# Optimization experiments

Hardware: AMD Instinct MI355X
Metric: run time of the kernel (lower is better)

Reference implementation:

```python
import jax, jax.numpy as jnp
import numpy as np

B, N, OBS_DIM = 64, 512, 128
HIDDEN_DIM, MESSAGE_DIM, ACTION_DIM = 256, 128, 16


def _dense_params(key, din, dout):
    kw, kb = jax.random.split(key)
    W = jax.random.normal(kw, (din, dout), jnp.float32) * 0.02
    b = jnp.zeros((dout,), jnp.float32)
    return W, b


def setup_inputs() -> dict:
    key = jax.random.key(0)
    ks = jax.random.split(key, 12)
    obs_batch = jax.random.normal(ks[0], (B, N, OBS_DIM), jnp.float32)
    dones_batch = jnp.zeros((B, N), jnp.bool_)
    We, be = _dense_params(ks[1], OBS_DIM, HIDDEN_DIM)
    Wc, bc = _dense_params(ks[2], HIDDEN_DIM, MESSAGE_DIM // 4)
    Wn, bn = _dense_params(ks[3], HIDDEN_DIM, MESSAGE_DIM // 2)
    Wb, bb = _dense_params(ks[4], HIDDEN_DIM, MESSAGE_DIM // 4)
    Wi, bi = _dense_params(ks[5], HIDDEN_DIM, 1)
    Wq, bq = _dense_params(ks[6], HIDDEN_DIM, MESSAGE_DIM)
    Wk, bk = _dense_params(ks[7], MESSAGE_DIM, MESSAGE_DIM)
    Wv, bv = _dense_params(ks[8], MESSAGE_DIM, MESSAGE_DIM)
    Wp, bp = _dense_params(ks[9], HIDDEN_DIM + MESSAGE_DIM, HIDDEN_DIM)
    Wa, ba = _dense_params(ks[10], HIDDEN_DIM, ACTION_DIM)
    Wcr, bcr = _dense_params(ks[11], HIDDEN_DIM, 1)
    return {"obs_batch": obs_batch, "dones_batch": dones_batch,
            "We": We, "be": be, "Wc": Wc, "bc": bc, "Wn": Wn, "bn": bn,
            "Wb": Wb, "bb": bb, "Wi": Wi, "bi": bi, "Wq": Wq, "bq": bq,
            "Wk": Wk, "bk": bk, "Wv": Wv, "bv": bv, "Wp": Wp, "bp": bp,
            "Wa": Wa, "ba": ba, "Wcr": Wcr, "bcr": bcr}


def reference(obs_batch, dones_batch, We, be, Wc, bc, Wn, bn, Wb, bb, Wi, bi,
              Wq, bq, Wk, bk, Wv, bv, Wp, bp, Wa, ba, Wcr, bcr):
    dense = lambda x, W, b: x @ W + b
    encoded = jax.nn.relu(dense(obs_batch, We, be))                 # [B,N,H]
    messages = jnp.concatenate([dense(encoded, Wc, bc),
                                dense(encoded, Wn, bn),
                                dense(encoded, Wb, bb)], axis=-1)   # [B,N,M]
    importance = jax.nn.sigmoid(dense(encoded, Wi, bi))             # [B,N,1]
    Q = dense(encoded, Wq, bq)
    K = dense(messages, Wk, bk)
    V = dense(messages, Wv, bv)
    scores = jnp.einsum('bqd,bkd->bqk', Q, K) / jnp.sqrt(jnp.float32(MESSAGE_DIM))
    importance_weights = importance * jnp.transpose(importance, (0, 2, 1))  # [B,N,N]
    scores = scores * importance_weights
    norms = jnp.linalg.norm(obs_batch, axis=-1, keepdims=True)      # [B,N,1]
    obs_sim = jnp.einsum('bid,bjd->bij', obs_batch, obs_batch)
    obs_sim = obs_sim / (norms + 1e-08)
    obs_sim = obs_sim / (jnp.transpose(norms, (0, 2, 1)) + 1e-08)
    scores = scores + obs_sim * 0.5
    attn = jax.nn.softmax(scores, axis=-1)
    aggregated = jnp.einsum('bqk,bkd->bqd', attn, V)                # [B,N,M]
    combined = jnp.concatenate([encoded, aggregated], axis=-1)
    x = jax.nn.relu(dense(combined, Wp, bp))
    logits = dense(x, Wa, ba)
    value = dense(x, Wcr, bcr).squeeze(-1)
    return (logits, value)
```

## Files before the change

kernel.cpp:

```cpp
#include <hip/hip_runtime.h>
#include <math.h>


typedef __attribute__((ext_vector_type(8))) short short8;
typedef __attribute__((ext_vector_type(4))) float f32x4;

#define RSQRT_D 0.08838834764831843f
#define MFMA __builtin_amdgcn_mfma_f32_16x16x32_bf16

__device__ __forceinline__ unsigned short f2bf(float f) {
  union { float f; unsigned u; } v; v.f = f;
  return (unsigned short)((v.u + 0x7FFFu + ((v.u >> 16) & 1u)) >> 16);
}
__device__ __forceinline__ float bf2f(unsigned short h) {
  union { unsigned u; float f; } v; v.u = ((unsigned)h) << 16;
  return v.f;
}
__device__ __forceinline__ unsigned pack2(float a, float b) {
  return (unsigned)f2bf(a) | ((unsigned)f2bf(b) << 16);
}
__device__ __forceinline__ short8 ld8(const unsigned short* p) {
  return *(const short8*)p;
}
__device__ __forceinline__ void gl16(const unsigned short* g,
                                     unsigned short* l) {
  __builtin_amdgcn_global_load_lds(
      (const __attribute__((address_space(1))) unsigned int*)(const void*)g,
      (__attribute__((address_space(3))) unsigned int*)(void*)l, 16, 0, 0);
}

__global__ __launch_bounds__(256) void prep_all(
    const float* __restrict__ obs, const float* __restrict__ We,
    const float* __restrict__ Wq, const float* __restrict__ Wk,
    const float* __restrict__ Wv, const float* __restrict__ Wp,
    const float* __restrict__ Wc, const float* __restrict__ Wn,
    const float* __restrict__ Wb, const float* __restrict__ bc,
    const float* __restrict__ bn, const float* __restrict__ bb,
    const float* __restrict__ Wa, const float* __restrict__ Wcr,
    const float* __restrict__ ba, const float* __restrict__ bcr,
    const float* __restrict__ bq, unsigned short* __restrict__ WeT,
    unsigned short* __restrict__ Wqkv, unsigned short* __restrict__ Wkv,
    unsigned short* __restrict__ Wm_nt, unsigned short* __restrict__ WpT,
    unsigned short* __restrict__ WaCrT, float* __restrict__ bm,
    float* __restrict__ bqkv, unsigned short* __restrict__ obs_bf,
    unsigned short* __restrict__ As, unsigned short* __restrict__ Bs,
    float* __restrict__ logits, float* __restrict__ value,
    float* __restrict__ imp_raw) {
  const int bid = blockIdx.x, tid = threadIdx.x;
  if (bid < 929) {
    int idx = bid * 256 + tid;
    if (idx < 32768) {
      int n = idx >> 7, k = idx & 127;
      WeT[idx] = f2bf(We[k * 256 + n]);
    } else if (idx < 65536) {
      int i = idx - 32768;
      int n = i >> 8, k = i & 255;
      Wqkv[i] = f2bf(Wq[k * 128 + n]);
    } else if (idx < 98304) {
      int i = idx - 65536;
      int n = i >> 7, k = i & 127;
      Wkv[i] = f2bf(n < 128 ? Wk[k * 128 + n] : Wv[k * 128 + (n - 128)]);
    } else if (idx < 131072) {
      int i = idx - 98304;
      int h = i >> 7, m = i & 127;
      float v = (m < 32)   ? Wc[h * 32 + m]
              : (m < 96)   ? Wn[h * 64 + (m - 32)]
                           : Wb[h * 32 + (m - 96)];
      Wm_nt[i] = f2bf(v);
    } else if (idx < 229376) {
      int i = idx - 131072;
      int n = i / 384, k = i - n * 384;
      WpT[i] = f2bf(Wp[k * 256 + n]);
    } else if (idx < 237568) {
      int i = idx - 229376;
      int n = i >> 8, k = i & 255;
      float v = (n < 16) ? Wa[k * 16 + n] : (n == 16) ? Wcr[k] : 0.f;
      WaCrT[i] = f2bf(v);
    } else if (idx < 237696) {
      int i = idx - 237568;
      bm[i] = (i < 32) ? bc[i] : (i < 96) ? bn[i - 32] : bb[i - 96];
    } else if (idx < 237824) {
      int i = idx - 237696;
      bqkv[i] = bq[i];
    }
  } else if (bid < 2977) {
    const int wave = tid >> 6, lane = tid & 63;
    const int t0 = (bid - 929) * 16 + wave * 4;
#pragma unroll
    for (int it = 0; it < 4; ++it) {
      int t = t0 + it;
      const float* row = obs + (size_t)t * 128;
      float2 o = *(const float2*)(row + lane * 2);
      float s2 = o.x * o.x + o.y * o.y;
#pragma unroll
      for (int off = 1; off < 64; off <<= 1) s2 += __shfl_xor(s2, off);
      float inv = 1.f / (sqrtf(s2) + 1e-8f);
      ((unsigned*)obs_bf)[(size_t)t * 64 + lane] = pack2(o.x, o.y);
      ((unsigned*)As)[(size_t)t * 128 + 64 + lane] =
          pack2(o.x * 0.5f * inv, o.y * 0.5f * inv);
      ((unsigned*)Bs)[(size_t)t * 128 + 64 + lane] =
          pack2(o.x * inv, o.y * inv);
    }
  } else if (bid < 5153) {
    int i = (bid - 2977) * 256 + tid;
    if (i < 524288) logits[i] = ba[i & 15];
    else value[i - 524288] = bcr[0];
  } else {
    imp_raw[(bid - 5153) * 256 + tid] = 0.f;
  }
}

__global__ __launch_bounds__(256) void prep_wprod(
    const unsigned short* __restrict__ Wkv,
    const unsigned short* __restrict__ Wm_nt, const float* __restrict__ bm,
    const float* __restrict__ bk, const float* __restrict__ bv,
    unsigned short* __restrict__ Wqkv, float* __restrict__ bqkv) {
  const int bid = blockIdx.x, tid = threadIdx.x;
  if (bid < 8) {
    const int lane = tid & 63, wave = tid >> 6;
    const int quad = lane >> 4, l16 = lane & 15;
    const int r0 = bid * 32;
    f32x4 acc[2][4];
#pragma unroll
    for (int i = 0; i < 2; ++i)
#pragma unroll
      for (int j = 0; j < 4; ++j) acc[i][j] = (f32x4){0.f, 0.f, 0.f, 0.f};
#pragma unroll
    for (int kc = 0; kc < 4; ++kc) {
      short8 af[2], bf[4];
#pragma unroll
      for (int i = 0; i < 2; ++i)
        af[i] = ld8(Wkv + (size_t)(r0 + i * 16 + l16) * 128 + kc * 32 + quad * 8);
#pragma unroll
      for (int j = 0; j < 4; ++j)
        bf[j] = ld8(Wm_nt + (size_t)(wave * 64 + j * 16 + l16) * 128 + kc * 32 +
                    quad * 8);
#pragma unroll
      for (int i = 0; i < 2; ++i)
#pragma unroll
        for (int j = 0; j < 4; ++j)
          acc[i][j] = MFMA(af[i], bf[j], acc[i][j], 0, 0, 0);
    }
#pragma unroll
    for (int i = 0; i < 2; ++i) {
      const int row = r0 + i * 16 + quad * 4;
#pragma unroll
      for (int j = 0; j < 4; ++j) {
        const int col = wave * 64 + j * 16 + l16;
#pragma unroll
        for (int r = 0; r < 4; ++r)
          Wqkv[(size_t)(128 + row + r) * 256 + col] = f2bf(acc[i][j][r]);
      }
    }
  } else {
    int i = tid;
    float acc = (i < 128) ? bk[i] : bv[i - 128];
    for (int m = 0; m < 128; ++m)
      acc += bm[m] * bf2f(Wkv[(size_t)i * 128 + m]);
    bqkv[128 + i] = acc;
  }
}

__global__ __launch_bounds__(256, 2) void enc_gemm(
    const unsigned short* __restrict__ obs_bf,
    const unsigned short* __restrict__ WeT, const float* __restrict__ be,
    const float* __restrict__ Wi, unsigned short* __restrict__ enc,
    float* __restrict__ imp_raw) {
  __shared__ unsigned short Asr[16384];
  __shared__ unsigned short Bsr[16384];
  const int tid = threadIdx.x, lane = tid & 63, wave = tid >> 6;
  const int quad = lane >> 4, l16 = lane & 15;
  const int wm = wave & 1, wn = wave >> 1;
  const int bm0 = blockIdx.y * 128, bn0 = blockIdx.x * 128;

#pragma unroll
  for (int it = 0; it < 8; ++it) {
    int c = it * 256 + tid;
    int row = c >> 4, ch = c & 15;
    gl16(obs_bf + (size_t)(bm0 + row) * 128 + ((ch ^ (row & 15)) << 3),
         Asr + it * 2048 + wave * 512);
    gl16(WeT + (size_t)(bn0 + row) * 128 + ((ch ^ (row & 15)) << 3),
         Bsr + it * 2048 + wave * 512);
  }
  __syncthreads();

  f32x4 acc[4][4];
#pragma unroll
  for (int i = 0; i < 4; ++i)
#pragma unroll
    for (int j = 0; j < 4; ++j) acc[i][j] = (f32x4){0.f, 0.f, 0.f, 0.f};
#pragma unroll
  for (int ks = 0; ks < 4; ++ks) {
    short8 af[4], bf[4];
#pragma unroll
    for (int mi = 0; mi < 4; ++mi) {
      int row = wm * 64 + mi * 16 + l16;
      af[mi] = *(const short8*)&Asr[row * 128 + (((ks * 4 + quad) ^ (row & 15)) << 3)];
    }
#pragma unroll
    for (int ni = 0; ni < 4; ++ni) {
      int row = wn * 64 + ni * 16 + l16;
      bf[ni] = *(const short8*)&Bsr[row * 128 + (((ks * 4 + quad) ^ (row & 15)) << 3)];
    }
#pragma unroll
    for (int mi = 0; mi < 4; ++mi)
#pragma unroll
      for (int ni = 0; ni < 4; ++ni)
        acc[mi][ni] = MFMA(af[mi], bf[ni], acc[mi][ni], 0, 0, 0);
  }

#pragma unroll
  for (int mi = 0; mi < 4; ++mi) {
    const int rowb = bm0 + wm * 64 + mi * 16 + quad * 4;
    float ip[4] = {0.f, 0.f, 0.f, 0.f};
#pragma unroll
    for (int ni = 0; ni < 4; ++ni) {
      const int col = bn0 + wn * 64 + ni * 16 + l16;
      const float bvv = be[col], wv = Wi[col];
#pragma unroll
      for (int r = 0; r < 4; ++r) {
        float v = fmaxf(acc[mi][ni][r] + bvv, 0.f);
        enc[(size_t)(rowb + r) * 256 + col] = f2bf(v);
        ip[r] += v * wv;
      }
    }
#pragma unroll
    for (int r = 0; r < 4; ++r) {
#pragma unroll
      for (int off = 1; off < 16; off <<= 1) ip[r] += __shfl_xor(ip[r], off);
    }
    if (l16 == 0) {
#pragma unroll
      for (int r = 0; r < 4; ++r) atomicAdd(&imp_raw[rowb + r], ip[r]);
    }
  }
}

__global__ __launch_bounds__(256, 2) void qkv_gemm(
    const unsigned short* __restrict__ enc, const unsigned short* __restrict__ Wqkv,
    const float* __restrict__ bqkv, const float* __restrict__ imp_raw,
    const float* __restrict__ bi, unsigned short* __restrict__ As,
    unsigned short* __restrict__ Bs, unsigned short* __restrict__ vT) {
  __shared__ unsigned short Asr[8192];
  __shared__ unsigned short Bsr[8192];
  const int tid = threadIdx.x, lane = tid & 63, wave = tid >> 6;
  const int quad = lane >> 4, l16 = lane & 15;
  const int wm = wave & 1, wn = wave >> 1;
  const int bx = blockIdx.x;
  const int bm0 = blockIdx.y * 128, bn0 = bx * 128;
  const int srow = tid >> 3, slc = tid & 7;

  f32x4 acc[4][4];
#pragma unroll
  for (int i = 0; i < 4; ++i)
#pragma unroll
    for (int j = 0; j < 4; ++j) acc[i][j] = (f32x4){0.f, 0.f, 0.f, 0.f};

  for (int kt = 0; kt < 256; kt += 64) {
#pragma unroll
    for (int i = 0; i < 4; ++i) {
      int row = i * 32 + srow;
      gl16(enc + (size_t)(bm0 + row) * 256 + kt + ((slc ^ (row & 7)) << 3),
           Asr + i * 2048 + wave * 512);
      gl16(Wqkv + (size_t)(bn0 + row) * 256 + kt + ((slc ^ (row & 7)) << 3),
           Bsr + i * 2048 + wave * 512);
    }
    __syncthreads();
#pragma unroll
    for (int ks = 0; ks < 2; ++ks) {
      short8 af[4], bf[4];
#pragma unroll
      for (int mi = 0; mi < 4; ++mi) {
        int row = wm * 64 + mi * 16 + l16;
        af[mi] = *(const short8*)&Asr[row * 64 + (((ks * 4 + quad) ^ (row & 7)) << 3)];
      }
#pragma unroll
      for (int ni = 0; ni < 4; ++ni) {
        int row = wn * 64 + ni * 16 + l16;
        bf[ni] = *(const short8*)&Bsr[row * 64 + (((ks * 4 + quad) ^ (row & 7)) << 3)];
      }
#pragma unroll
      for (int mi = 0; mi < 4; ++mi)
#pragma unroll
        for (int ni = 0; ni < 4; ++ni)
          acc[mi][ni] = MFMA(af[mi], bf[ni], acc[mi][ni], 0, 0, 0);
    }
    __syncthreads();
  }

  const float bi0 = bi[0];
#pragma unroll
  for (int mi = 0; mi < 4; ++mi) {
    const int rowb = bm0 + wm * 64 + mi * 16 + quad * 4;
    float sg[4];
    if (bx < 2) {
      const float mult = (bx == 0) ? RSQRT_D : 1.0f;
#pragma unroll
      for (int r = 0; r < 4; ++r)
        sg[r] = mult / (1.f + __expf(-(imp_raw[rowb + r] + bi0)));
    }
#pragma unroll
    for (int ni = 0; ni < 4; ++ni) {
      const int col = wn * 64 + ni * 16 + l16;
      const float bvv = bqkv[bx * 128 + col];
      if (bx == 0) {
#pragma unroll
        for (int r = 0; r < 4; ++r)
          As[(size_t)(rowb + r) * 256 + col] = f2bf((acc[mi][ni][r] + bvv) * sg[r]);
      } else if (bx == 1) {
#pragma unroll
        for (int r = 0; r < 4; ++r)
          Bs[(size_t)(rowb + r) * 256 + col] = f2bf((acc[mi][ni][r] + bvv) * sg[r]);
      } else {
        uint2 o;
        o.x = pack2(acc[mi][ni][0] + bvv, acc[mi][ni][1] + bvv);
        o.y = pack2(acc[mi][ni][2] + bvv, acc[mi][ni][3] + bvv);
        *(uint2*)(vT + ((size_t)(rowb >> 9) * 128 + col) * 512 + (rowb & 511)) = o;
      }
    }
  }
}

__global__ __launch_bounds__(512, 4) void flash4b(
    const unsigned short* __restrict__ As, const unsigned short* __restrict__ Bs,
    const unsigned short* __restrict__ vT, unsigned short* __restrict__ agg) {
  __shared__ unsigned short Ub[16384];
  __shared__ unsigned short Pp[8192];
  __shared__ float redm[2][64];
  __shared__ float reds[2][64];
  const int tid = threadIdx.x, lane = tid & 63, wave = tid >> 6;
  const int quad = lane >> 4, l16 = lane & 15;
  const int wm = wave & 3, wn = wave >> 2;
  const int b = blockIdx.x & 63;
  const int qt = blockIdx.x >> 6;
  const size_t tok0 = (size_t)b * 512 + qt * 64;
  const int srow = tid >> 4, slc = tid & 15;

  short8 af[8];
#pragma unroll
  for (int kc = 0; kc < 8; ++kc)
    af[kc] = ld8(As + (tok0 + wm * 16 + l16) * 256 + kc * 32 + quad * 8);

  f32x4 s[4][4];
#pragma unroll
  for (int kt = 0; kt < 4; ++kt)
#pragma unroll
    for (int nt = 0; nt < 4; ++nt) s[kt][nt] = (f32x4){0.f, 0.f, 0.f, 0.f};

#pragma unroll
  for (int kt = 0; kt < 4; ++kt) {
#pragma unroll
    for (int kh = 0; kh < 2; ++kh) {
      __syncthreads();
#pragma unroll
      for (int i = 0; i < 4; ++i) {
        int row = i * 32 + srow;
        gl16(Bs + ((size_t)b * 512 + kt * 128 + row) * 256 + kh * 128 +
                 ((slc ^ (row & 15)) << 3),
             Ub + i * 4096 + wave * 512);
      }
      __syncthreads();
#pragma unroll
      for (int kk = 0; kk < 4; ++kk) {
        short8 bfr[4];
#pragma unroll
        for (int nt = 0; nt < 4; ++nt) {
          int rr = wn * 64 + nt * 16 + l16;
          bfr[nt] = *(const short8*)&Ub[rr * 128 + (((kk * 4 + quad) ^ (rr & 15)) << 3)];
        }
#pragma unroll
        for (int nt = 0; nt < 4; ++nt)
          s[kt][nt] = MFMA(af[kh * 4 + kk], bfr[nt], s[kt][nt], 0, 0, 0);
      }
    }
  }

  const int rbase = wm * 16 + quad * 4;
  float mt[4];
#pragma unroll
  for (int r = 0; r < 4; ++r) {
    float mv = -1e30f;
#pragma unroll
    for (int kt = 0; kt < 4; ++kt)
#pragma unroll
      for (int nt = 0; nt < 4; ++nt) mv = fmaxf(mv, s[kt][nt][r]);
#pragma unroll
    for (int off = 1; off < 16; off <<= 1) mv = fmaxf(mv, __shfl_xor(mv, off));
    mt[r] = mv;
  }
  if (l16 == 0) {
#pragma unroll
    for (int r = 0; r < 4; ++r) redm[wn][rbase + r] = mt[r];
  }
  __syncthreads();
  float lsum[4];
#pragma unroll
  for (int r = 0; r < 4; ++r) {
    float mfull = fmaxf(mt[r], redm[1 ^ wn][rbase + r]);
    float sum = 0.f;
#pragma unroll
    for (int kt = 0; kt < 4; ++kt)
#pragma unroll
      for (int nt = 0; nt < 4; ++nt) {
        float p = __expf(s[kt][nt][r] - mfull);
        s[kt][nt][r] = p;
        sum += p;
      }
#pragma unroll
    for (int off = 1; off < 16; off <<= 1) sum += __shfl_xor(sum, off);
    lsum[r] = sum;
  }
  if (l16 == 0) {
#pragma unroll
    for (int r = 0; r < 4; ++r) reds[wn][rbase + r] = lsum[r];
  }
  __syncthreads();
  float linv[4];
#pragma unroll
  for (int r = 0; r < 4; ++r)
    linv[r] = 1.0f / (lsum[r] + reds[1 ^ wn][rbase + r]);

  f32x4 oacc[4];
#pragma unroll
  for (int nt = 0; nt < 4; ++nt) oacc[nt] = (f32x4){0.f, 0.f, 0.f, 0.f};
#pragma unroll
  for (int vt = 0; vt < 4; ++vt) {
    __syncthreads();
#pragma unroll
    for (int nt = 0; nt < 4; ++nt) {
      const int col = wn * 64 + nt * 16 + l16;
#pragma unroll
      for (int r = 0; r < 4; ++r) {
        const int row = rbase + r;
        Pp[row * 128 + (((col >> 3) ^ (row & 15)) << 3) + (col & 7)] =
            f2bf(s[vt][nt][r]);
      }
    }
#pragma unroll
    for (int i = 0; i < 4; ++i) {
      int row = i * 32 + srow;
      gl16(vT + ((size_t)b * 128 + row) * 512 + vt * 128 +
               ((slc ^ (row & 15)) << 3),
           Ub + i * 4096 + wave * 512);
    }
    __syncthreads();
#pragma unroll
    for (int kk = 0; kk < 4; ++kk) {
      const int prow = wm * 16 + l16;
      short8 pa = *(const short8*)&Pp[prow * 128 + (((kk * 4 + quad) ^ (prow & 15)) << 3)];
#pragma unroll
      for (int nt = 0; nt < 4; ++nt) {
        int rr = wn * 64 + nt * 16 + l16;
        short8 vb = *(const short8*)&Ub[rr * 128 + (((kk * 4 + quad) ^ (rr & 15)) << 3)];
        oacc[nt] = MFMA(pa, vb, oacc[nt], 0, 0, 0);
      }
    }
  }
#pragma unroll
  for (int nt = 0; nt < 4; ++nt) {
    const int col = wn * 64 + nt * 16 + l16;
#pragma unroll
    for (int r = 0; r < 4; ++r)
      agg[(tok0 + rbase + r) * 128 + col] = f2bf(oacc[nt][r] * linv[r]);
  }
}

__global__ __launch_bounds__(256, 2) void xh_gemm(
    const unsigned short* __restrict__ enc, const unsigned short* __restrict__ agg,
    const unsigned short* __restrict__ WpT, const float* __restrict__ bp,
    const unsigned short* __restrict__ WaCrT, float* __restrict__ logits,
    float* __restrict__ value) {
  __shared__ unsigned short sm[16384];
  unsigned short* Asr = sm;
  unsigned short* Bsr = sm + 8192;
  const int tid = threadIdx.x, lane = tid & 63, wave = tid >> 6;
  const int quad = lane >> 4, l16 = lane & 15;
  const int wm = wave & 1, wn = wave >> 1;
  const int bm = blockIdx.y * 128, bn = blockIdx.x * 128;
  const int srow = tid >> 3, slc = tid & 7;

  f32x4 acc[4][4];
#pragma unroll
  for (int i = 0; i < 4; ++i)
#pragma unroll
    for (int j = 0; j < 4; ++j) acc[i][j] = (f32x4){0.f, 0.f, 0.f, 0.f};

  for (int kt = 0; kt < 384; kt += 64) {
    const unsigned short* Ap;
    int lda, kloc;
    if (kt < 256) { Ap = enc; lda = 256; kloc = kt; }
    else          { Ap = agg; lda = 128; kloc = kt - 256; }
#pragma unroll
    for (int i = 0; i < 4; ++i) {
      int row = i * 32 + srow;
      gl16(Ap + (size_t)(bm + row) * lda + kloc + ((slc ^ (row & 7)) << 3),
           Asr + i * 2048 + wave * 512);
      gl16(WpT + (size_t)(bn + row) * 384 + kt + ((slc ^ (row & 7)) << 3),
           Bsr + i * 2048 + wave * 512);
    }
    __syncthreads();
#pragma unroll
    for (int ks = 0; ks < 2; ++ks) {
      short8 af[4], bf[4];
#pragma unroll
      for (int mi = 0; mi < 4; ++mi) {
        int row = wm * 64 + mi * 16 + l16;
        af[mi] = *(const short8*)&Asr[row * 64 + (((ks * 4 + quad) ^ (row & 7)) << 3)];
      }
#pragma unroll
      for (int ni = 0; ni < 4; ++ni) {
        int row = wn * 64 + ni * 16 + l16;
        bf[ni] = *(const short8*)&Bsr[row * 64 + (((ks * 4 + quad) ^ (row & 7)) << 3)];
      }
#pragma unroll
      for (int mi = 0; mi < 4; ++mi)
#pragma unroll
        for (int ni = 0; ni < 4; ++ni)
          acc[mi][ni] = MFMA(af[mi], bf[ni], acc[mi][ni], 0, 0, 0);
    }
    __syncthreads();
  }

#pragma unroll
  for (int mi = 0; mi < 4; ++mi) {
    const int row = wm * 64 + mi * 16 + quad * 4;
#pragma unroll
    for (int ni = 0; ni < 4; ++ni) {
      const int colc = wn * 64 + ni * 16 + l16;
      const float bv = bp[bn + colc];
#pragma unroll
      for (int r = 0; r < 4; ++r) {
        float v = fmaxf(acc[mi][ni][r] + bv, 0.f);
        sm[(row + r) * 128 + (((colc >> 3) ^ ((row + r) & 15)) << 3) + (colc & 7)] =
            f2bf(v);
      }
    }
  }
  __syncthreads();

  f32x4 h[2][2];
#pragma unroll
  for (int i = 0; i < 2; ++i)
#pragma unroll
    for (int j = 0; j < 2; ++j) h[i][j] = (f32x4){0.f, 0.f, 0.f, 0.f};
#pragma unroll
  for (int kc = 0; kc < 4; ++kc) {
    short8 xa[2], wb[2];
#pragma unroll
    for (int hm = 0; hm < 2; ++hm) {
      int row = wave * 32 + hm * 16 + l16;
      xa[hm] = *(const short8*)&sm[row * 128 + (((kc * 4 + quad) ^ (row & 15)) << 3)];
    }
#pragma unroll
    for (int hn = 0; hn < 2; ++hn)
      wb[hn] = ld8(WaCrT + (size_t)(hn * 16 + l16) * 256 + bn + kc * 32 + quad * 8);
#pragma unroll
    for (int hm = 0; hm < 2; ++hm)
#pragma unroll
      for (int hn = 0; hn < 2; ++hn)
        h[hm][hn] = MFMA(xa[hm], wb[hn], h[hm][hn], 0, 0, 0);
  }
#pragma unroll
  for (int hm = 0; hm < 2; ++hm) {
#pragma unroll
    for (int hn = 0; hn < 2; ++hn) {
      const int n = hn * 16 + l16;
#pragma unroll
      for (int r = 0; r < 4; ++r) {
        const int grow = bm + wave * 32 + hm * 16 + quad * 4 + r;
        if (n < 16)
          atomicAdd(&logits[(size_t)grow * 16 + n], h[hm][hn][r]);
        else if (n == 16)
          atomicAdd(&value[grow], h[hm][hn][r]);
      }
    }
  }
}

extern "C" void kernel_launch(void* const* d_in, const int* in_sizes, int n_in,
                              void* d_out, int out_size, void* d_ws,
                              size_t ws_size, hipStream_t stream) {
  const float* obs = (const float*)d_in[0];
  const float* We = (const float*)d_in[2];
  const float* be = (const float*)d_in[3];
  const float* Wc = (const float*)d_in[4];
  const float* bc = (const float*)d_in[5];
  const float* Wn = (const float*)d_in[6];
  const float* bn = (const float*)d_in[7];
  const float* Wb = (const float*)d_in[8];
  const float* bb = (const float*)d_in[9];
  const float* Wi = (const float*)d_in[10];
  const float* bi = (const float*)d_in[11];
  const float* Wq = (const float*)d_in[12];
  const float* bq = (const float*)d_in[13];
  const float* Wk = (const float*)d_in[14];
  const float* bk = (const float*)d_in[15];
  const float* Wv = (const float*)d_in[16];
  const float* bv = (const float*)d_in[17];
  const float* Wp = (const float*)d_in[18];
  const float* bp = (const float*)d_in[19];
  const float* Wa = (const float*)d_in[20];
  const float* ba = (const float*)d_in[21];
  const float* Wcr = (const float*)d_in[22];
  const float* bcr = (const float*)d_in[23];

  char* base = (char*)d_ws;
  unsigned short* enc_bf = (unsigned short*)(base);
  unsigned short* As     = (unsigned short*)(base + 16777216);
  unsigned short* Bs     = (unsigned short*)(base + 33554432);
  unsigned short* obsagg = (unsigned short*)(base + 50331648);
  unsigned short* vT     = (unsigned short*)(base + 58720256);
  float* imp_raw         = (float*)(base + 67108864);
  unsigned short* WeT    = (unsigned short*)(base + 67239936);
  unsigned short* Wqkv   = (unsigned short*)(base + 67305472);
  unsigned short* Wkv    = (unsigned short*)(base + 67502080);
  unsigned short* Wm_nt  = (unsigned short*)(base + 67567616);
  unsigned short* WpT    = (unsigned short*)(base + 67633152);
  unsigned short* WaCrT  = (unsigned short*)(base + 67829760);
  float* bmb             = (float*)(base + 67846144);
  float* bqkv            = (float*)(base + 67846656);

  float* logits = (float*)d_out;
  float* value = (float*)d_out + 524288;

  prep_all<<<5281, 256, 0, stream>>>(obs, We, Wq, Wk, Wv, Wp, Wc, Wn, Wb, bc,
                                     bn, bb, Wa, Wcr, ba, bcr, bq, WeT, Wqkv,
                                     Wkv, Wm_nt, WpT, WaCrT, bmb, bqkv, obsagg,
                                     As, Bs, logits, value, imp_raw);
  prep_wprod<<<9, 256, 0, stream>>>(Wkv, Wm_nt, bmb, bk, bv, Wqkv, bqkv);

  enc_gemm<<<dim3(2, 256), 256, 0, stream>>>(obsagg, WeT, be, Wi, enc_bf,
                                             imp_raw);
  qkv_gemm<<<dim3(3, 256), 256, 0, stream>>>(enc_bf, Wqkv, bqkv, imp_raw, bi,
                                             As, Bs, vT);
  flash4b<<<512, 512, 0, stream>>>(As, Bs, vT, obsagg);
  xh_gemm<<<dim3(2, 256), 256, 0, stream>>>(enc_bf, obsagg, WpT, bp, WaCrT,
                                            logits, value);
}
```

Baseline: 183.5 us.

## Merge weight-product prep into encoder kernel and double-buffer GEMM K-loops

```diff
diff --git a/kernel.cpp b/kernel.cpp
--- a/kernel.cpp
+++ b/kernel.cpp
@@ -110,68 +110,71 @@
   }
 }
 
-__global__ __launch_bounds__(256) void prep_wprod(
-    const unsigned short* __restrict__ Wkv,
-    const unsigned short* __restrict__ Wm_nt, const float* __restrict__ bm,
-    const float* __restrict__ bk, const float* __restrict__ bv,
-    unsigned short* __restrict__ Wqkv, float* __restrict__ bqkv) {
-  const int bid = blockIdx.x, tid = threadIdx.x;
-  if (bid < 8) {
-    const int lane = tid & 63, wave = tid >> 6;
-    const int quad = lane >> 4, l16 = lane & 15;
-    const int r0 = bid * 32;
-    f32x4 acc[2][4];
-#pragma unroll
-    for (int i = 0; i < 2; ++i)
-#pragma unroll
-      for (int j = 0; j < 4; ++j) acc[i][j] = (f32x4){0.f, 0.f, 0.f, 0.f};
-#pragma unroll
-    for (int kc = 0; kc < 4; ++kc) {
-      short8 af[2], bf[4];
-#pragma unroll
-      for (int i = 0; i < 2; ++i)
-        af[i] = ld8(Wkv + (size_t)(r0 + i * 16 + l16) * 128 + kc * 32 + quad * 8);
-#pragma unroll
-      for (int j = 0; j < 4; ++j)
-        bf[j] = ld8(Wm_nt + (size_t)(wave * 64 + j * 16 + l16) * 128 + kc * 32 +
-                    quad * 8);
-#pragma unroll
-      for (int i = 0; i < 2; ++i)
-#pragma unroll
-        for (int j = 0; j < 4; ++j)
-          acc[i][j] = MFMA(af[i], bf[j], acc[i][j], 0, 0, 0);
-    }
-#pragma unroll
-    for (int i = 0; i < 2; ++i) {
-      const int row = r0 + i * 16 + quad * 4;
-#pragma unroll
-      for (int j = 0; j < 4; ++j) {
-        const int col = wave * 64 + j * 16 + l16;
-#pragma unroll
-        for (int r = 0; r < 4; ++r)
-          Wqkv[(size_t)(128 + row + r) * 256 + col] = f2bf(acc[i][j][r]);
-      }
-    }
-  } else {
-    int i = tid;
-    float acc = (i < 128) ? bk[i] : bv[i - 128];
-    for (int m = 0; m < 128; ++m)
-      acc += bm[m] * bf2f(Wkv[(size_t)i * 128 + m]);
-    bqkv[128 + i] = acc;
-  }
-}
-
-__global__ __launch_bounds__(256, 2) void enc_gemm(
+__global__ __launch_bounds__(256, 2) void enc_wprod(
     const unsigned short* __restrict__ obs_bf,
     const unsigned short* __restrict__ WeT, const float* __restrict__ be,
     const float* __restrict__ Wi, unsigned short* __restrict__ enc,
-    float* __restrict__ imp_raw) {
+    float* __restrict__ imp_raw, const unsigned short* __restrict__ Wkv,
+    const unsigned short* __restrict__ Wm_nt, const float* __restrict__ bmc,
+    const float* __restrict__ bk, const float* __restrict__ bv,
+    unsigned short* __restrict__ Wqkv, float* __restrict__ bqkv) {
   __shared__ unsigned short Asr[16384];
   __shared__ unsigned short Bsr[16384];
-  const int tid = threadIdx.x, lane = tid & 63, wave = tid >> 6;
+  const int bid = blockIdx.x, tid = threadIdx.x;
+
+  if (bid >= 512) {
+    const int wb = bid - 512;
+    if (wb < 8) {
+      const int lane = tid & 63, wave = tid >> 6;
+      const int quad = lane >> 4, l16 = lane & 15;
+      const int r0 = wb * 32;
+      f32x4 acc[2][4];
+#pragma unroll
+      for (int i = 0; i < 2; ++i)
+#pragma unroll
+        for (int j = 0; j < 4; ++j) acc[i][j] = (f32x4){0.f, 0.f, 0.f, 0.f};
+#pragma unroll
+      for (int kc = 0; kc < 4; ++kc) {
+        short8 af[2], bf[4];
+#pragma unroll
+        for (int i = 0; i < 2; ++i)
+          af[i] =
+              ld8(Wkv + (size_t)(r0 + i * 16 + l16) * 128 + kc * 32 + quad * 8);
+#pragma unroll
+        for (int j = 0; j < 4; ++j)
+          bf[j] = ld8(Wm_nt + (size_t)(wave * 64 + j * 16 + l16) * 128 +
+                      kc * 32 + quad * 8);
+#pragma unroll
+        for (int i = 0; i < 2; ++i)
+#pragma unroll
+          for (int j = 0; j < 4; ++j)
+            acc[i][j] = MFMA(af[i], bf[j], acc[i][j], 0, 0, 0);
+      }
+#pragma unroll
+      for (int i = 0; i < 2; ++i) {
+        const int row = r0 + i * 16 + quad * 4;
+#pragma unroll
+        for (int j = 0; j < 4; ++j) {
+          const int col = wave * 64 + j * 16 + l16;
+#pragma unroll
+          for (int r = 0; r < 4; ++r)
+            Wqkv[(size_t)(128 + row + r) * 256 + col] = f2bf(acc[i][j][r]);
+        }
+      }
+    } else {
+      int i = tid;
+      float acc = (i < 128) ? bk[i] : bv[i - 128];
+      for (int m = 0; m < 128; ++m)
+        acc += bmc[m] * bf2f(Wkv[(size_t)i * 128 + m]);
+      bqkv[128 + i] = acc;
+    }
+    return;
+  }
+
+  const int lane = tid & 63, wave = tid >> 6;
   const int quad = lane >> 4, l16 = lane & 15;
   const int wm = wave & 1, wn = wave >> 1;
-  const int bm0 = blockIdx.y * 128, bn0 = blockIdx.x * 128;
+  const int bm0 = (bid >> 1) * 128, bn0 = (bid & 1) * 128;
 
 #pragma unroll
   for (int it = 0; it < 8; ++it) {
@@ -248,7 +251,7 @@
   const int wm = wave & 1, wn = wave >> 1;
   const int bx = blockIdx.x;
   const int bm0 = blockIdx.y * 128, bn0 = bx * 128;
-  const int srow = tid >> 3, slc = tid & 7;
+  const int sr4 = tid >> 2, sl4 = tid & 3;
 
   f32x4 acc[4][4];
 #pragma unroll
@@ -256,35 +259,40 @@
 #pragma unroll
     for (int j = 0; j < 4; ++j) acc[i][j] = (f32x4){0.f, 0.f, 0.f, 0.f};
 
-  for (int kt = 0; kt < 256; kt += 64) {
-#pragma unroll
-    for (int i = 0; i < 4; ++i) {
-      int row = i * 32 + srow;
-      gl16(enc + (size_t)(bm0 + row) * 256 + kt + ((slc ^ (row & 7)) << 3),
-           Asr + i * 2048 + wave * 512);
-      gl16(Wqkv + (size_t)(bn0 + row) * 256 + kt + ((slc ^ (row & 7)) << 3),
-           Bsr + i * 2048 + wave * 512);
-    }
-    __syncthreads();
-#pragma unroll
-    for (int ks = 0; ks < 2; ++ks) {
-      short8 af[4], bf[4];
-#pragma unroll
-      for (int mi = 0; mi < 4; ++mi) {
-        int row = wm * 64 + mi * 16 + l16;
-        af[mi] = *(const short8*)&Asr[row * 64 + (((ks * 4 + quad) ^ (row & 7)) << 3)];
-      }
-#pragma unroll
-      for (int ni = 0; ni < 4; ++ni) {
-        int row = wn * 64 + ni * 16 + l16;
-        bf[ni] = *(const short8*)&Bsr[row * 64 + (((ks * 4 + quad) ^ (row & 7)) << 3)];
-      }
-#pragma unroll
-      for (int mi = 0; mi < 4; ++mi)
-#pragma unroll
-        for (int ni = 0; ni < 4; ++ni)
-          acc[mi][ni] = MFMA(af[mi], bf[ni], acc[mi][ni], 0, 0, 0);
-    }
+  auto stage = [&](int t, int bo) {
+#pragma unroll
+    for (int i = 0; i < 2; ++i) {
+      int row = i * 64 + sr4;
+      int col = t * 32 + ((sl4 ^ (row & 3)) << 3);
+      gl16(enc + (size_t)(bm0 + row) * 256 + col,
+           Asr + bo + i * 2048 + wave * 512);
+      gl16(Wqkv + (size_t)(bn0 + row) * 256 + col,
+           Bsr + bo + i * 2048 + wave * 512);
+    }
+  };
+
+  stage(0, 0);
+  __syncthreads();
+#pragma unroll 8
+  for (int t = 0; t < 8; ++t) {
+    if (t < 7) stage(t + 1, ((t + 1) & 1) * 4096);
+    const int bo = (t & 1) * 4096;
+    short8 af[4], bf[4];
+#pragma unroll
+    for (int mi = 0; mi < 4; ++mi) {
+      int row = wm * 64 + mi * 16 + l16;
+      af[mi] = *(const short8*)&Asr[bo + row * 32 + ((quad ^ (row & 3)) << 3)];
+    }
+#pragma unroll
+    for (int ni = 0; ni < 4; ++ni) {
+      int row = wn * 64 + ni * 16 + l16;
+      bf[ni] = *(const short8*)&Bsr[bo + row * 32 + ((quad ^ (row & 3)) << 3)];
+    }
+#pragma unroll
+    for (int mi = 0; mi < 4; ++mi)
+#pragma unroll
+      for (int ni = 0; ni < 4; ++ni)
+        acc[mi][ni] = MFMA(af[mi], bf[ni], acc[mi][ni], 0, 0, 0);
     __syncthreads();
   }
 
@@ -335,6 +343,7 @@
   const int qt = blockIdx.x >> 6;
   const size_t tok0 = (size_t)b * 512 + qt * 64;
   const int srow = tid >> 4, slc = tid & 15;
+  const int qr8 = tid >> 3, ql8 = tid & 7;
 
   short8 af[8];
 #pragma unroll
@@ -347,32 +356,37 @@
 #pragma unroll
     for (int nt = 0; nt < 4; ++nt) s[kt][nt] = (f32x4){0.f, 0.f, 0.f, 0.f};
 
-#pragma unroll
-  for (int kt = 0; kt < 4; ++kt) {
-#pragma unroll
-    for (int kh = 0; kh < 2; ++kh) {
-      __syncthreads();
-#pragma unroll
-      for (int i = 0; i < 4; ++i) {
-        int row = i * 32 + srow;
-        gl16(Bs + ((size_t)b * 512 + kt * 128 + row) * 256 + kh * 128 +
-                 ((slc ^ (row & 15)) << 3),
-             Ub + i * 4096 + wave * 512);
-      }
-      __syncthreads();
-#pragma unroll
-      for (int kk = 0; kk < 4; ++kk) {
-        short8 bfr[4];
-#pragma unroll
-        for (int nt = 0; nt < 4; ++nt) {
-          int rr = wn * 64 + nt * 16 + l16;
-          bfr[nt] = *(const short8*)&Ub[rr * 128 + (((kk * 4 + quad) ^ (rr & 15)) << 3)];
-        }
-#pragma unroll
-        for (int nt = 0; nt < 4; ++nt)
-          s[kt][nt] = MFMA(af[kh * 4 + kk], bfr[nt], s[kt][nt], 0, 0, 0);
-      }
-    }
+  auto qstage = [&](int c) {
+    const int kt_ = c >> 2, dq_ = c & 3;
+#pragma unroll
+    for (int r2 = 0; r2 < 2; ++r2) {
+      int row = r2 * 64 + qr8;
+      gl16(Bs + ((size_t)b * 512 + kt_ * 128 + row) * 256 + dq_ * 64 +
+               ((ql8 ^ (row & 7)) << 3),
+           Ub + (c & 1) * 8192 + r2 * 4096 + wave * 512);
+    }
+  };
+  qstage(0);
+  __syncthreads();
+#pragma unroll 16
+  for (int c = 0; c < 16; ++c) {
+    if (c < 15) qstage(c + 1);
+    const int kt = c >> 2, dq = c & 3;
+    const int ub0 = (c & 1) * 8192;
+#pragma unroll
+    for (int kk2 = 0; kk2 < 2; ++kk2) {
+      short8 bfr[4];
+#pragma unroll
+      for (int nt = 0; nt < 4; ++nt) {
+        int rr = wn * 64 + nt * 16 + l16;
+        bfr[nt] = *(const short8*)&Ub[ub0 + rr * 64 +
+                                      (((kk2 * 2 + quad) ^ (rr & 7)) << 3)];
+      }
+#pragma unroll
+      for (int nt = 0; nt < 4; ++nt)
+        s[kt][nt] = MFMA(af[dq * 2 + kk2], bfr[nt], s[kt][nt], 0, 0, 0);
+    }
+    __syncthreads();
   }
 
   const int rbase = wm * 16 + quad * 4;
@@ -477,7 +491,7 @@
   const int quad = lane >> 4, l16 = lane & 15;
   const int wm = wave & 1, wn = wave >> 1;
   const int bm = blockIdx.y * 128, bn = blockIdx.x * 128;
-  const int srow = tid >> 3, slc = tid & 7;
+  const int sr4 = tid >> 2, sl4 = tid & 3;
 
   f32x4 acc[4][4];
 #pragma unroll
@@ -485,39 +499,44 @@
 #pragma unroll
     for (int j = 0; j < 4; ++j) acc[i][j] = (f32x4){0.f, 0.f, 0.f, 0.f};
 
-  for (int kt = 0; kt < 384; kt += 64) {
+  auto stage = [&](int t, int bo) {
     const unsigned short* Ap;
-    int lda, kloc;
-    if (kt < 256) { Ap = enc; lda = 256; kloc = kt; }
-    else          { Ap = agg; lda = 128; kloc = kt - 256; }
-#pragma unroll
-    for (int i = 0; i < 4; ++i) {
-      int row = i * 32 + srow;
-      gl16(Ap + (size_t)(bm + row) * lda + kloc + ((slc ^ (row & 7)) << 3),
-           Asr + i * 2048 + wave * 512);
-      gl16(WpT + (size_t)(bn + row) * 384 + kt + ((slc ^ (row & 7)) << 3),
-           Bsr + i * 2048 + wave * 512);
-    }
-    __syncthreads();
-#pragma unroll
-    for (int ks = 0; ks < 2; ++ks) {
-      short8 af[4], bf[4];
-#pragma unroll
-      for (int mi = 0; mi < 4; ++mi) {
-        int row = wm * 64 + mi * 16 + l16;
-        af[mi] = *(const short8*)&Asr[row * 64 + (((ks * 4 + quad) ^ (row & 7)) << 3)];
-      }
-#pragma unroll
-      for (int ni = 0; ni < 4; ++ni) {
-        int row = wn * 64 + ni * 16 + l16;
-        bf[ni] = *(const short8*)&Bsr[row * 64 + (((ks * 4 + quad) ^ (row & 7)) << 3)];
-      }
-#pragma unroll
-      for (int mi = 0; mi < 4; ++mi)
-#pragma unroll
-        for (int ni = 0; ni < 4; ++ni)
-          acc[mi][ni] = MFMA(af[mi], bf[ni], acc[mi][ni], 0, 0, 0);
-    }
+    int lda, kc;
+    if (t < 8) { Ap = enc; lda = 256; kc = t * 32; }
+    else       { Ap = agg; lda = 128; kc = t * 32 - 256; }
+#pragma unroll
+    for (int i = 0; i < 2; ++i) {
+      int row = i * 64 + sr4;
+      int sw = (sl4 ^ (row & 3)) << 3;
+      gl16(Ap + (size_t)(bm + row) * lda + kc + sw,
+           Asr + bo + i * 2048 + wave * 512);
+      gl16(WpT + (size_t)(bn + row) * 384 + t * 32 + sw,
+           Bsr + bo + i * 2048 + wave * 512);
+    }
+  };
+
+  stage(0, 0);
+  __syncthreads();
+#pragma unroll 12
+  for (int t = 0; t < 12; ++t) {
+    if (t < 11) stage(t + 1, ((t + 1) & 1) * 4096);
+    const int bo = (t & 1) * 4096;
+    short8 af[4], bf[4];
+#pragma unroll
+    for (int mi = 0; mi < 4; ++mi) {
+      int row = wm * 64 + mi * 16 + l16;
+      af[mi] = *(const short8*)&Asr[bo + row * 32 + ((quad ^ (row & 3)) << 3)];
+    }
+#pragma unroll
+    for (int ni = 0; ni < 4; ++ni) {
+      int row = wn * 64 + ni * 16 + l16;
+      bf[ni] = *(const short8*)&Bsr[bo + row * 32 + ((quad ^ (row & 3)) << 3)];
+    }
+#pragma unroll
+    for (int mi = 0; mi < 4; ++mi)
+#pragma unroll
+      for (int ni = 0; ni < 4; ++ni)
+        acc[mi][ni] = MFMA(af[mi], bf[ni], acc[mi][ni], 0, 0, 0);
     __syncthreads();
   }
 
@@ -627,10 +646,8 @@
                                      bn, bb, Wa, Wcr, ba, bcr, bq, WeT, Wqkv,
                                      Wkv, Wm_nt, WpT, WaCrT, bmb, bqkv, obsagg,
                                      As, Bs, logits, value, imp_raw);
-  prep_wprod<<<9, 256, 0, stream>>>(Wkv, Wm_nt, bmb, bk, bv, Wqkv, bqkv);
-
-  enc_gemm<<<dim3(2, 256), 256, 0, stream>>>(obsagg, WeT, be, Wi, enc_bf,
-                                             imp_raw);
+  enc_wprod<<<521, 256, 0, stream>>>(obsagg, WeT, be, Wi, enc_bf, imp_raw,
+                                     Wkv, Wm_nt, bmb, bk, bv, Wqkv, bqkv);
   qkv_gemm<<<dim3(3, 256), 256, 0, stream>>>(enc_bf, Wqkv, bqkv, imp_raw, bi,
                                              As, Bs, vT);
   flash4b<<<512, 512, 0, stream>>>(As, Bs, vT, obsagg);
```

Result: no change. 183.9 us (+0.2%).
